# Kernel tuning notes

Measured on AMD Instinct MI355X. Metric: run time of the kernel, lower is better.

The kernel has to match this reference:

```python
import jax, jax.numpy as jnp
import numpy as np

BSZ, SEQ, EMBED, HEADS = 2, 2048, 1024, 16
HEAD_DIM = EMBED // HEADS


def setup_inputs() -> dict:
    key = jax.random.key(0)
    ks = jax.random.split(key, 12)
    s = 0.02
    inp = {
        'query': jax.random.normal(ks[0], (BSZ, SEQ, EMBED), jnp.float32),
        'key':   jax.random.normal(ks[1], (BSZ, SEQ, EMBED), jnp.float32),
        'value': jax.random.normal(ks[2], (BSZ, SEQ, EMBED), jnp.float32),
        # causal mask, broadcast over batch: positions with 0 are masked to -inf
        'mask': jnp.broadcast_to(jnp.tril(jnp.ones((SEQ, SEQ), jnp.int32)), (BSZ, SEQ, SEQ)),
        'Wq': jax.random.normal(ks[3], (EMBED, EMBED), jnp.float32) * s,
        'bq': jnp.zeros((EMBED,), jnp.float32),
        'Wk': jax.random.normal(ks[4], (EMBED, EMBED), jnp.float32) * s,
        'bk': jnp.zeros((EMBED,), jnp.float32),
        'Wv': jax.random.normal(ks[5], (EMBED, EMBED), jnp.float32) * s,
        'bv': jnp.zeros((EMBED,), jnp.float32),
        'Wo': jax.random.normal(ks[6], (EMBED, EMBED), jnp.float32) * s,
        'bo': jnp.zeros((EMBED,), jnp.float32),
    }
    return inp


def reference(query, key, value, mask, Wq, bq, Wk, bk, Wv, bv, Wo, bo):
    bsz, seq_len, embed_dim = query.shape
    scaling = HEAD_DIM ** -0.5

    def proj(x, W, b):  # torch Linear: x @ W.T + b, then split heads -> [b, h, s, d]
        y = jnp.einsum('bse,fe->bsf', x, W) + b
        return y.reshape(bsz, -1, HEADS, HEAD_DIM).transpose(0, 2, 1, 3)

    q = proj(query, Wq, bq)
    k = proj(key, Wk, bk)
    v = proj(value, Wv, bv)

    scores = jnp.einsum('bhqd,bhkd->bhqk', q, k) * scaling  # [b, h, s, s]
    scores = jnp.where(mask[:, None, :, :] == 0, -jnp.inf, scores)
    attn = jax.nn.softmax(scores, axis=-1)  # dropout p=0.0 -> identity
    vals = jnp.einsum('bhqk,bhkd->bhqd', attn, v)
    vals = vals.transpose(0, 2, 1, 3).reshape(bsz, seq_len, embed_dim)
    out = jnp.einsum('bse,fe->bsf', vals, Wo) + bo
    return out
```

## Files before the change

### kernel.cpp

```cpp
#include <hip/hip_runtime.h>
#include <hip/hip_bf16.h>


typedef __bf16 bf16;
typedef bf16 bf16x4 __attribute__((ext_vector_type(4)));
typedef bf16 bf16x8 __attribute__((ext_vector_type(8)));
typedef float f32x4 __attribute__((ext_vector_type(4)));

constexpr int BSZ = 2, SEQ = 2048, EMBED = 1024, HEADS = 16, HDIM = 64;
constexpr int MTOT = BSZ * SEQ;
constexpr int KDIM = EMBED;
constexpr float QSCALE = 0.125f * 1.4426950408889634f;

constexpr size_t XSZ = (size_t)MTOT * EMBED;
constexpr size_t WSZ = (size_t)EMBED * EMBED;

__device__ inline void load_lds16(const bf16* g, bf16* l) {
    __builtin_amdgcn_global_load_lds(
        (const __attribute__((address_space(1))) unsigned int*)g,
        (__attribute__((address_space(3))) unsigned int*)l, 16, 0, 0);
}

__global__ __launch_bounds__(256) void cvt_bf16(
    const float* __restrict__ x0, const float* __restrict__ x1, const float* __restrict__ x2,
    const float* __restrict__ w0, const float* __restrict__ w1,
    const float* __restrict__ w2, const float* __restrict__ w3,
    bf16* __restrict__ dst) {
    const size_t i = ((size_t)blockIdx.x * blockDim.x + threadIdx.x) * 8;
    const float* src;
    size_t off;
    if (i < 3 * XSZ) {
        const int s = (int)(i >> 22);
        src = s == 0 ? x0 : (s == 1 ? x1 : x2);
        off = i & (XSZ - 1);
    } else {
        const size_t j = i - 3 * XSZ;
        const int s = (int)(j >> 20);
        src = s == 0 ? w0 : (s == 1 ? w1 : (s == 2 ? w2 : w3));
        off = j & (WSZ - 1);
    }
    float4 a = *(const float4*)(src + off);
    float4 b = *(const float4*)(src + off + 4);
    bf16x8 v = {(bf16)a.x, (bf16)a.y, (bf16)a.z, (bf16)a.w,
                (bf16)b.x, (bf16)b.y, (bf16)b.z, (bf16)b.w};
    *(bf16x8*)(dst + i) = v;
}

struct MMCtx {
    int wave, lane, quad, l16, wm, wn, lrow, lcol;
};
__device__ inline MMCtx mm_ctx() {
    MMCtx c;
    const int tid = threadIdx.x;
    c.wave = tid >> 6; c.lane = tid & 63;
    c.quad = c.lane >> 4; c.l16 = c.lane & 15;
    c.wm = (c.wave & 1) * 64; c.wn = (c.wave >> 1) * 64;
    c.lrow = c.lane >> 3; c.lcol = (c.lane & 7) * 8;
    return c;
}

template <bool SWAP>
__device__ inline void mm_loop(const bf16* __restrict__ A, const bf16* __restrict__ W,
                               int rowA0, int rowB0, const MMCtx& c,
                               bf16 (*As)[64], bf16 (*Bs)[64], f32x4 acc[4][4]) {
    for (int k0 = 0; k0 < KDIM; k0 += 64) {
        for (int i = 0; i < 4; ++i) {
            const int r0 = (c.wave * 4 + i) * 8;
            load_lds16(&A[(size_t)(rowA0 + r0 + c.lrow) * KDIM + k0 + c.lcol], &As[r0][0]);
            load_lds16(&W[(size_t)(rowB0 + r0 + c.lrow) * KDIM + k0 + c.lcol], &Bs[r0][0]);
        }
        __syncthreads();
        for (int ks = 0; ks < 64; ks += 32) {
            bf16x8 af[4], bfr[4];
            for (int mt = 0; mt < 4; ++mt)
                af[mt] = *(const bf16x8*)&As[c.wm + mt * 16 + c.l16][ks + c.quad * 8];
            for (int nt = 0; nt < 4; ++nt)
                bfr[nt] = *(const bf16x8*)&Bs[c.wn + nt * 16 + c.l16][ks + c.quad * 8];
            for (int mt = 0; mt < 4; ++mt)
                for (int nt = 0; nt < 4; ++nt)
                    acc[mt][nt] = SWAP
                        ? __builtin_amdgcn_mfma_f32_16x16x32_bf16(bfr[nt], af[mt], acc[mt][nt], 0, 0, 0)
                        : __builtin_amdgcn_mfma_f32_16x16x32_bf16(af[mt], bfr[nt], acc[mt][nt], 0, 0, 0);
        }
        __syncthreads();
    }
}

__global__ __launch_bounds__(256) void gemm_qkv(
    const bf16* __restrict__ Xq, const bf16* __restrict__ Xk, const bf16* __restrict__ Xv,
    const bf16* __restrict__ Wq, const bf16* __restrict__ Wk, const bf16* __restrict__ Wv,
    const float* __restrict__ bq, const float* __restrict__ bk, const float* __restrict__ bv,
    bf16* __restrict__ Qp, bf16* __restrict__ Kp, bf16* __restrict__ Vtp) {
    __shared__ bf16 As[128][64];
    __shared__ bf16 Bs[128][64];

    const int z = blockIdx.z;
    const bf16* A     = z == 0 ? Xq : (z == 1 ? Xk : Xv);
    const bf16* W     = z == 0 ? Wq : (z == 1 ? Wk : Wv);
    const float* bias = z == 0 ? bq : (z == 1 ? bk : bv);
    const float scale = z == 0 ? QSCALE : 1.0f;

    const MMCtx c = mm_ctx();
    const int rowA0 = blockIdx.x * 128;
    const int rowB0 = blockIdx.y * 128;
    f32x4 acc[4][4] = {};

    if (z < 2) {
        mm_loop<true>(A, W, rowA0, rowB0, c, As, Bs, acc);
        bf16* dst = z == 0 ? Qp : Kp;
        for (int mt = 0; mt < 4; ++mt) {
            const int xrow = rowA0 + c.wm + mt * 16 + c.l16;
            const int b = xrow >> 11, s = xrow & (SEQ - 1);
            for (int nt = 0; nt < 4; ++nt) {
                const int f0 = rowB0 + c.wn + nt * 16 + c.quad * 4;
                const float4 bb = *(const float4*)&bias[f0];
                const int h = f0 >> 6, d0 = f0 & (HDIM - 1);
                f32x4 a = acc[mt][nt];
                bf16x4 pk = {(bf16)((a[0] + bb.x) * scale), (bf16)((a[1] + bb.y) * scale),
                             (bf16)((a[2] + bb.z) * scale), (bf16)((a[3] + bb.w) * scale)};
                *(bf16x4*)&dst[(((size_t)(b * HEADS + h)) * SEQ + s) * HDIM + d0] = pk;
            }
        }
    } else {
        mm_loop<false>(A, W, rowA0, rowB0, c, As, Bs, acc);
        for (int nt = 0; nt < 4; ++nt) {
            const int f = rowB0 + c.wn + nt * 16 + c.l16;
            const float bb = bias[f];
            const int h = f >> 6, d = f & (HDIM - 1);
            for (int mt = 0; mt < 4; ++mt) {
                const int xrow0 = rowA0 + c.wm + mt * 16 + c.quad * 4;
                const int b = xrow0 >> 11, s0 = xrow0 & (SEQ - 1);
                f32x4 a = acc[mt][nt];
                bf16x4 pk = {(bf16)(a[0] + bb), (bf16)(a[1] + bb),
                             (bf16)(a[2] + bb), (bf16)(a[3] + bb)};
                *(bf16x4*)&Vtp[(((size_t)(b * HEADS + h)) * HDIM + d) * SEQ + s0] = pk;
            }
        }
    }
}

__global__ __launch_bounds__(256) void gemm_out(const bf16* __restrict__ A,
                                                const bf16* __restrict__ W,
                                                const float* __restrict__ bias,
                                                float* __restrict__ C) {
    __shared__ bf16 As[128][64];
    __shared__ bf16 Bs[64][64];

    const int tid = threadIdx.x;
    const int wave = tid >> 6, lane = tid & 63;
    const int quad = lane >> 4, l16 = lane & 15;
    const int wm = (wave & 1) * 64, wn = (wave >> 1) * 32;
    const int lrow = lane >> 3, lcol = (lane & 7) * 8;
    const int rowA0 = blockIdx.x * 128;
    const int rowB0 = blockIdx.y * 64;

    f32x4 acc[4][2] = {};
    for (int k0 = 0; k0 < KDIM; k0 += 64) {
        for (int i = 0; i < 4; ++i) {
            const int r0 = (wave * 4 + i) * 8;
            load_lds16(&A[(size_t)(rowA0 + r0 + lrow) * KDIM + k0 + lcol], &As[r0][0]);
        }
        {
            const int r0 = wave * 16 + (lane >> 2) * 2;
        }
        for (int i = 0; i < 2; ++i) {
            const int r0 = (wave * 2 + i) * 8;
            load_lds16(&W[(size_t)(rowB0 + r0 + lrow) * KDIM + k0 + lcol], &Bs[r0][0]);
        }
        __syncthreads();
        for (int ks = 0; ks < 64; ks += 32) {
            bf16x8 af[4], bfr[2];
            for (int mt = 0; mt < 4; ++mt)
                af[mt] = *(const bf16x8*)&As[wm + mt * 16 + l16][ks + quad * 8];
            for (int nt = 0; nt < 2; ++nt)
                bfr[nt] = *(const bf16x8*)&Bs[wn + nt * 16 + l16][ks + quad * 8];
            for (int mt = 0; mt < 4; ++mt)
                for (int nt = 0; nt < 2; ++nt)
                    acc[mt][nt] = __builtin_amdgcn_mfma_f32_16x16x32_bf16(
                        bfr[nt], af[mt], acc[mt][nt], 0, 0, 0);
        }
        __syncthreads();
    }

    for (int mt = 0; mt < 4; ++mt) {
        const int row = rowA0 + wm + mt * 16 + l16;
        for (int nt = 0; nt < 2; ++nt) {
            const int f0 = rowB0 + wn + nt * 16 + quad * 4;
            const float4 bb = *(const float4*)&bias[f0];
            f32x4 a = acc[mt][nt];
            float4 v = {a[0] + bb.x, a[1] + bb.y, a[2] + bb.z, a[3] + bb.w};
            *(float4*)&C[(size_t)row * EMBED + f0] = v;
        }
    }
}

__global__ __launch_bounds__(256) void attn_flash(const bf16* __restrict__ Q,
                                                  const bf16* __restrict__ K,
                                                  const bf16* __restrict__ Vt,
                                                  bf16* __restrict__ O) {
    const int bh = blockIdx.y;
    const int pair = blockIdx.x;
    const int wave = threadIdx.x >> 6, lane = threadIdx.x & 63;
    const int quad = lane >> 4, l16 = lane & 15;

    const bf16* Qh = Q + (size_t)bh * SEQ * HDIM;
    const bf16* Kh = K + (size_t)bh * SEQ * HDIM;
    const bf16* Vh = Vt + (size_t)bh * HDIM * SEQ;

    __shared__ bf16 Ks[2][64][64];
    __shared__ bf16 Vs[2][64][64];
    __shared__ bf16 Ps[4][16][72];

    const int srow = wave * 8 + (lane >> 3);
    const int scolL = (lane & 7) * 8;
    const int b = bh >> 4, h = bh & 15;

    auto stage = [&](int buf, int k0) {
        for (int cc = 0; cc < 2; ++cc) {
            const int row = srow + cc * 32;
            const int gcol = (scolL - 8 * row) & 63;
            load_lds16(&Kh[(size_t)(k0 + row) * HDIM + gcol], &Ks[buf][wave * 8 + cc * 32][0]);
            load_lds16(&Vh[(size_t)row * SEQ + k0 + gcol], &Vs[buf][wave * 8 + cc * 32][0]);
        }
    };

#pragma unroll 1
    for (int phase = 0; phase < 2; ++phase) {
        const int qt = phase == 0 ? (31 - pair) : pair;
        const int qb = qt * 64;
        const int qw = qb + wave * 16;
        const int nk = qt + 1;

        bf16x8 qf[2];
        for (int ks = 0; ks < 2; ++ks)
            qf[ks] = *(const bf16x8*)&Qh[(size_t)(qw + l16) * HDIM + ks * 32 + quad * 8];

        f32x4 ot[4] = {};
        float lsum = 0.f;

        stage(0, 0);
#pragma unroll 1
        for (int it = 0; it < nk; ++it) {
            const int k0 = it * 64;
            const int buf = it & 1;
            __syncthreads();
            if (it + 1 < nk) stage(buf ^ 1, k0 + 64);

            if (k0 < qw + 16) {
                f32x4 st[4] = {};
                for (int mt = 0; mt < 4; ++mt) {
                    const int krow = mt * 16 + l16;
                    for (int ks = 0; ks < 2; ++ks) {
                        const int colL = (ks * 32 + 8 * (quad + krow)) & 63;
                        bf16x8 kf = *(const bf16x8*)&Ks[buf][krow][colL];
                        st[mt] = __builtin_amdgcn_mfma_f32_16x16x32_bf16(kf, qf[ks], st[mt], 0, 0, 0);
                    }
                }
                if (k0 + 63 >= qw) {
                    const int q = qw + l16;
                    for (int mt = 0; mt < 4; ++mt) {
                        const int key = k0 + mt * 16 + quad * 4;
                        for (int r = 0; r < 4; ++r)
                            if (key + r > q) st[mt][r] = -__builtin_inff();
                    }
                }
                for (int mt = 0; mt < 4; ++mt) {
                    f32x4 p;
                    for (int r = 0; r < 4; ++r) p[r] = exp2f(st[mt][r]);
                    lsum += p[0] + p[1] + p[2] + p[3];
                    bf16x4 pk = {(bf16)p[0], (bf16)p[1], (bf16)p[2], (bf16)p[3]};
                    *(bf16x4*)&Ps[wave][l16][mt * 16 + quad * 4] = pk;
                }
                for (int half = 0; half < 2; ++half) {
                    bf16x8 pf = *(const bf16x8*)&Ps[wave][l16][half * 32 + quad * 8];
                    for (int dt = 0; dt < 4; ++dt) {
                        const int drow = dt * 16 + l16;
                        const int colL = (half * 32 + 8 * (quad + drow)) & 63;
                        bf16x8 vf = *(const bf16x8*)&Vs[buf][drow][colL];
                        ot[dt] = __builtin_amdgcn_mfma_f32_16x16x32_bf16(vf, pf, ot[dt], 0, 0, 0);
                    }
                }
            }
        }
        __syncthreads();

        float l = lsum;
        l += __shfl_xor(l, 16);
        l += __shfl_xor(l, 32);
        const float inv = 1.f / l;
        const int sq = qw + l16;
        for (int dt = 0; dt < 4; ++dt) {
            bf16x4 pk = {(bf16)(ot[dt][0] * inv), (bf16)(ot[dt][1] * inv),
                         (bf16)(ot[dt][2] * inv), (bf16)(ot[dt][3] * inv)};
            *(bf16x4*)&O[((size_t)(b * SEQ + sq)) * EMBED + h * HDIM + dt * 16 + quad * 4] = pk;
        }
    }
}

extern "C" void kernel_launch(void* const* d_in, const int* in_sizes, int n_in,
                              void* d_out, int out_size, void* d_ws, size_t ws_size,
                              hipStream_t stream) {
    const float* q_in = (const float*)d_in[0];
    const float* k_in = (const float*)d_in[1];
    const float* v_in = (const float*)d_in[2];
    const float* Wq = (const float*)d_in[4];
    const float* bq = (const float*)d_in[5];
    const float* Wk = (const float*)d_in[6];
    const float* bk = (const float*)d_in[7];
    const float* Wv = (const float*)d_in[8];
    const float* bv = (const float*)d_in[9];
    const float* Wo = (const float*)d_in[10];
    const float* bo = (const float*)d_in[11];

    bf16* ws = (bf16*)d_ws;
    bf16* Xb  = ws;
    bf16* Wb  = ws + 3 * XSZ;
    bf16* Qp  = ws + 3 * XSZ + 4 * WSZ;
    bf16* Kp  = Qp + XSZ;
    bf16* Vtp = Kp + XSZ;
    bf16* AO  = ws;

    const size_t total = 3 * XSZ + 4 * WSZ;
    dim3 bb(256);
    cvt_bf16<<<dim3((unsigned)(total / 8 / 256)), bb, 0, stream>>>(
        q_in, k_in, v_in, Wq, Wk, Wv, Wo, ws);
    gemm_qkv<<<dim3(MTOT / 128, EMBED / 128, 3), bb, 0, stream>>>(
        Xb, Xb + XSZ, Xb + 2 * XSZ, Wb, Wb + WSZ, Wb + 2 * WSZ,
        bq, bk, bv, Qp, Kp, Vtp);
    attn_flash<<<dim3(16, BSZ * HEADS), bb, 0, stream>>>(Qp, Kp, Vtp, AO);
    gemm_out<<<dim3(MTOT / 128, EMBED / 64), bb, 0, stream>>>(
        AO, Wb + 3 * WSZ, bo, (float*)d_out);
}
```

Baseline: 257.7 us.

## Swizzle GEMM LDS tiles and remap attention block order across XCDs

Applies an XOR-free rotation swizzle to the LDS layout of the A and W tiles in both GEMM kernels. The global column fetched by each lane is rotated by row so that MFMA fragment reads from shared memory avoid bank conflicts. The attention kernel also remaps the linear block index so that consecutive blocks spread heads across the eight XCDs, which should keep the K/V of a head in one XCD's L2 and balance causal work. The cost is a little extra index arithmetic per load, and the remap's assumptions are tied to the grid shape.

After: 245.1 us. 4.9% less time.

```diff
diff --git a/kernel.cpp b/kernel.cpp
--- a/kernel.cpp
+++ b/kernel.cpp
@@ -66,16 +66,22 @@
     for (int k0 = 0; k0 < KDIM; k0 += 64) {
         for (int i = 0; i < 4; ++i) {
             const int r0 = (c.wave * 4 + i) * 8;
-            load_lds16(&A[(size_t)(rowA0 + r0 + c.lrow) * KDIM + k0 + c.lcol], &As[r0][0]);
-            load_lds16(&W[(size_t)(rowB0 + r0 + c.lrow) * KDIM + k0 + c.lcol], &Bs[r0][0]);
+            const int row = r0 + c.lrow;
+            const int gcol = (c.lcol - 8 * row) & 63;
+            load_lds16(&A[(size_t)(rowA0 + row) * KDIM + k0 + gcol], &As[r0][0]);
+            load_lds16(&W[(size_t)(rowB0 + row) * KDIM + k0 + gcol], &Bs[r0][0]);
         }
         __syncthreads();
         for (int ks = 0; ks < 64; ks += 32) {
             bf16x8 af[4], bfr[4];
-            for (int mt = 0; mt < 4; ++mt)
-                af[mt] = *(const bf16x8*)&As[c.wm + mt * 16 + c.l16][ks + c.quad * 8];
-            for (int nt = 0; nt < 4; ++nt)
-                bfr[nt] = *(const bf16x8*)&Bs[c.wn + nt * 16 + c.l16][ks + c.quad * 8];
+            for (int mt = 0; mt < 4; ++mt) {
+                const int row = c.wm + mt * 16 + c.l16;
+                af[mt] = *(const bf16x8*)&As[row][(ks + c.quad * 8 + 8 * row) & 63];
+            }
+            for (int nt = 0; nt < 4; ++nt) {
+                const int row = c.wn + nt * 16 + c.l16;
+                bfr[nt] = *(const bf16x8*)&Bs[row][(ks + c.quad * 8 + 8 * row) & 63];
+            }
             for (int mt = 0; mt < 4; ++mt)
                 for (int nt = 0; nt < 4; ++nt)
                     acc[mt][nt] = SWAP
@@ -158,22 +164,27 @@
     for (int k0 = 0; k0 < KDIM; k0 += 64) {
         for (int i = 0; i < 4; ++i) {
             const int r0 = (wave * 4 + i) * 8;
-            load_lds16(&A[(size_t)(rowA0 + r0 + lrow) * KDIM + k0 + lcol], &As[r0][0]);
-        }
-        {
-            const int r0 = wave * 16 + (lane >> 2) * 2;
+            const int row = r0 + lrow;
+            const int gcol = (lcol - 8 * row) & 63;
+            load_lds16(&A[(size_t)(rowA0 + row) * KDIM + k0 + gcol], &As[r0][0]);
         }
         for (int i = 0; i < 2; ++i) {
             const int r0 = (wave * 2 + i) * 8;
-            load_lds16(&W[(size_t)(rowB0 + r0 + lrow) * KDIM + k0 + lcol], &Bs[r0][0]);
+            const int row = r0 + lrow;
+            const int gcol = (lcol - 8 * row) & 63;
+            load_lds16(&W[(size_t)(rowB0 + row) * KDIM + k0 + gcol], &Bs[r0][0]);
         }
         __syncthreads();
         for (int ks = 0; ks < 64; ks += 32) {
             bf16x8 af[4], bfr[2];
-            for (int mt = 0; mt < 4; ++mt)
-                af[mt] = *(const bf16x8*)&As[wm + mt * 16 + l16][ks + quad * 8];
-            for (int nt = 0; nt < 2; ++nt)
-                bfr[nt] = *(const bf16x8*)&Bs[wn + nt * 16 + l16][ks + quad * 8];
+            for (int mt = 0; mt < 4; ++mt) {
+                const int row = wm + mt * 16 + l16;
+                af[mt] = *(const bf16x8*)&As[row][(ks + quad * 8 + 8 * row) & 63];
+            }
+            for (int nt = 0; nt < 2; ++nt) {
+                const int row = wn + nt * 16 + l16;
+                bfr[nt] = *(const bf16x8*)&Bs[row][(ks + quad * 8 + 8 * row) & 63];
+            }
             for (int mt = 0; mt < 4; ++mt)
                 for (int nt = 0; nt < 2; ++nt)
                     acc[mt][nt] = __builtin_amdgcn_mfma_f32_16x16x32_bf16(
@@ -198,8 +209,10 @@
                                                   const bf16* __restrict__ K,
                                                   const bf16* __restrict__ Vt,
                                                   bf16* __restrict__ O) {
-    const int bh = blockIdx.y;
-    const int pair = blockIdx.x;
+    const int l = blockIdx.x + (blockIdx.y << 4);
+    const int a = l & 7, s = l >> 3;
+    const int bh = 4 * a + (s >> 4);
+    const int pair = s & 15;
     const int wave = threadIdx.x >> 6, lane = threadIdx.x & 63;
     const int quad = lane >> 4, l16 = lane & 15;
 
@@ -284,10 +297,10 @@
         }
         __syncthreads();
 
-        float l = lsum;
-        l += __shfl_xor(l, 16);
-        l += __shfl_xor(l, 32);
-        const float inv = 1.f / l;
+        float l2 = lsum;
+        l2 += __shfl_xor(l2, 16);
+        l2 += __shfl_xor(l2, 32);
+        const float inv = 1.f / l2;
         const int sq = qw + l16;
         for (int dt = 0; dt < 4; ++dt) {
             bf16x4 pk = {(bf16)(ot[dt][0] * inv), (bf16)(ot[dt][1] * inv),
```
